# Performance work log

Measured on AMD Instinct MI355X. Metric: run time of the kernel, lower is better.

The kernel has to match this reference:

```python
import jax, jax.numpy as jnp
import numpy as np

N, E, D_IN, D, H = 50000, 600000, 128, 128, 128
NEG_SLOPE = 0.2  # PyG GATConv default


def setup_inputs() -> dict:
    key = jax.random.key(0)
    ks = jax.random.split(key, 10)
    s = 1.0 / np.sqrt(D)
    return {
        "x": jax.random.normal(ks[0], (N, D_IN), jnp.float32),
        "edge_index": jax.random.randint(ks[1], (2, E), 0, N, jnp.int64),
        "h": jax.random.normal(ks[2], (1, N, H), jnp.float32),
        "c": jax.random.normal(ks[3], (1, N, H), jnp.float32),
        "W": jax.random.normal(ks[4], (D_IN, D), jnp.float32) * s,
        "att_src": jax.random.normal(ks[5], (D,), jnp.float32) * s,
        "att_dst": jax.random.normal(ks[6], (D,), jnp.float32) * s,
        "bias_gat": jnp.zeros((D,), jnp.float32),
        "W_ih": jax.random.normal(ks[7], (4 * H, D), jnp.float32) * s,
        "W_hh": jax.random.normal(ks[8], (4 * H, H), jnp.float32) * s,
    }


def _gat_conv(x, edge_index, W, att_src, att_dst, bias_gat):
    n = x.shape[0]
    xs = x @ W  # [N, D]
    # add self loops (PyG default add_self_loops=True)
    loop = jnp.arange(n, dtype=edge_index.dtype)
    src = jnp.concatenate([edge_index[0], loop])
    dst = jnp.concatenate([edge_index[1], loop])
    a_src = xs @ att_src  # [N]
    a_dst = xs @ att_dst  # [N]
    e = a_src[src] + a_dst[dst]  # [E+N]
    e = jnp.where(e >= 0, e, NEG_SLOPE * e)  # leaky_relu
    # segment softmax over edges grouped by destination node
    e_max = jax.ops.segment_max(e, dst, num_segments=n)
    e_exp = jnp.exp(e - e_max[dst])
    e_sum = jax.ops.segment_sum(e_exp, dst, num_segments=n)
    alpha = e_exp / (e_sum[dst] + 1e-16)  # [E+N]
    out = jax.ops.segment_sum(alpha[:, None] * xs[src], dst, num_segments=n)
    return out + bias_gat


def _lstm_step(x, h0, c0, W_ih, W_hh):
    # torch LSTM gate order: i, f, g, o; bias=False
    gates = x @ W_ih.T + h0 @ W_hh.T  # [N, 4H]
    i, f, g, o = jnp.split(gates, 4, axis=-1)
    i, f, o = jax.nn.sigmoid(i), jax.nn.sigmoid(f), jax.nn.sigmoid(o)
    g = jnp.tanh(g)
    c1 = f * c0 + i * g
    h1 = o * jnp.tanh(c1)
    return h1, c1


def reference(x, edge_index, h, c, W, att_src, att_dst, bias_gat, W_ih, W_hh):
    xb = jnp.tanh(_gat_conv(x, edge_index, W, att_src, att_dst, bias_gat))  # [N, D]
    h1, c1 = _lstm_step(xb, h[0], c[0], W_ih, W_hh)
    # LSTM output for seq_len=1 equals the new hidden state
    return xb * 0 + h1, h1[None], c1[None]
```

## Files before the change

kernel.cpp:

```cpp
#include <hip/hip_runtime.h>
#include <hip/hip_bf16.h>
#include <math.h>

#define NEG 0.2f

typedef float f32x4 __attribute__((ext_vector_type(4)));
typedef short bf16x8 __attribute__((ext_vector_type(8)));

__device__ __forceinline__ float fsig(float x){ return 1.0f/(1.0f+__expf(-x)); }
__device__ __forceinline__ float ftanh(float x){ float e = __expf(2.0f*x); return 1.0f - 2.0f/(e+1.0f); }
__device__ __forceinline__ unsigned short f2bf(float v){
    __hip_bfloat16 b = __float2bfloat16(v);
    return *(unsigned short*)&b;
}
__device__ __forceinline__ bf16x8 pack8(float4 u, float4 v){
    bf16x8 r;
    r[0]=(short)f2bf(u.x); r[1]=(short)f2bf(u.y); r[2]=(short)f2bf(u.z); r[3]=(short)f2bf(u.w);
    r[4]=(short)f2bf(v.x); r[5]=(short)f2bf(v.y); r[6]=(short)f2bf(v.z); r[7]=(short)f2bf(v.w);
    return r;
}
__device__ __forceinline__ bf16x8 asbf(f32x4 v){ union{f32x4 f; bf16x8 h;} u; u.f=v; return u.h; }

__global__ void k_probe(const int* __restrict__ ei, int* __restrict__ flag){
    if(threadIdx.x==0){
        int nz=0;
        for(int i=0;i<64;i++) nz |= ei[2*i+1];
        *flag = (nz==0) ? 1 : 0;
    }
}

__global__ __launch_bounds__(256) void k_wpackx(const float* __restrict__ W,
                                                unsigned short* __restrict__ WPX){
    int f = blockIdx.x*256 + threadIdx.x;
    int l = f&63, ct = (f>>6)&7, ks = f>>9;
    int k0 = ks*32 + (l>>4)*8;
    int col = ct*16 + (l&15);
    #pragma unroll
    for(int j=0;j<8;j++) WPX[(size_t)f*8+j] = f2bf(W[(size_t)(k0+j)*128 + col]);
}

__global__ __launch_bounds__(256) void k_wtpack2(const float* __restrict__ W_ih,
                                                 const float* __restrict__ W_hh,
                                                 unsigned short* __restrict__ WP2){
    int f = blockIdx.x*256 + threadIdx.x;
    int l = f&63, ct = (f>>6)&3, ks = (f>>8)&7, g = f>>11;
    int k0 = ks*32 + (l>>4)*8;
    int col = ct*128 + g*16 + (l&15);
    #pragma unroll
    for(int j=0;j<8;j++){
        int k = k0+j;
        float w = (k<128) ? W_ih[(size_t)col*128+k] : W_hh[(size_t)col*128+(k-128)];
        WP2[(size_t)f*8+j] = f2bf(w);
    }
}

__global__ __launch_bounds__(256,2) void k_gemm_xs3(const float* __restrict__ x,
                                                    const unsigned short* __restrict__ WPX,
                                                    const float* __restrict__ att_s,
                                                    const float* __restrict__ att_d,
                                                    unsigned short* __restrict__ xsb,
                                                    float* __restrict__ a_src,
                                                    float* __restrict__ a_dst,
                                                    int n, int ntiles, int nwaves){
    const int w = threadIdx.x>>6, l = threadIdx.x&63;
    const int wid = blockIdx.x*4 + w;
    bf16x8 B[32];
    #pragma unroll
    for(int f=0;f<32;f++) B[f] = *(const bf16x8*)(WPX + (size_t)(f*64 + l)*8);
    float asv[8], adv[8];
    #pragma unroll
    for(int ct=0;ct<8;ct++){
        asv[ct] = att_s[ct*16 + (l&15)];
        adv[ct] = att_d[ct*16 + (l&15)];
    }
    for(int rt = wid; rt < ntiles; rt += nwaves){
        int arow = rt*16 + (l&15); if(arow>=n) arow = n-1;
        const float* xr = x + (size_t)arow*128 + (l>>4)*8;
        bf16x8 A[4];
        #pragma unroll
        for(int ks=0;ks<4;ks++){
            float4 u = *(const float4*)(xr + ks*32);
            float4 v = *(const float4*)(xr + ks*32 + 4);
            A[ks] = pack8(u,v);
        }
        f32x4 acc[8];
        #pragma unroll
        for(int ct=0;ct<8;ct++) acc[ct] = (f32x4){0.f,0.f,0.f,0.f};
        #pragma unroll
        for(int ks=0;ks<4;ks++){
            #pragma unroll
            for(int ct=0;ct<8;ct++)
                acc[ct] = __builtin_amdgcn_mfma_f32_16x16x32_bf16(A[ks], B[ks*8+ct], acc[ct], 0,0,0);
        }
        #pragma unroll
        for(int reg=0;reg<4;reg++){
            int row = rt*16 + (l>>4)*4 + reg;
            float ps=0.f, pd=0.f;
            #pragma unroll
            for(int ct=0;ct<8;ct++){ ps += acc[ct][reg]*asv[ct]; pd += acc[ct][reg]*adv[ct]; }
            ps += __shfl_xor(ps,1); pd += __shfl_xor(pd,1);
            ps += __shfl_xor(ps,2); pd += __shfl_xor(pd,2);
            ps += __shfl_xor(ps,4); pd += __shfl_xor(pd,4);
            ps += __shfl_xor(ps,8); pd += __shfl_xor(pd,8);
            if((l&15)==0 && row<n){ a_src[row]=ps; a_dst[row]=pd; }
            if(row<n){
                #pragma unroll
                for(int ct=0;ct<8;ct++)
                    xsb[(size_t)row*128 + ct*16 + (l&15)] = f2bf(acc[ct][reg]);
            }
        }
    }
}

__global__ __launch_bounds__(256) void k_hist(const int* __restrict__ ei,
                                              const int* __restrict__ flag,
                                              int* __restrict__ deg, int E, int EN){
    int e = blockIdx.x*256 + threadIdx.x;
    if(e>=EN) return;
    int dst = (e>=E) ? (e-E) : (*flag ? ei[2*(E+e)] : ei[E+e]);
    atomicAdd(&deg[dst], 1);
}

__global__ __launch_bounds__(256) void k_scan1(const int* __restrict__ deg,
                                               int* __restrict__ bsum, int n){
    __shared__ int ws[4];
    int b = blockIdx.x, t = threadIdx.x;
    int i = b*512 + t*2;
    int s = 0;
    if(i<n)   s += deg[i];
    if(i+1<n) s += deg[i+1];
    for(int off=32;off;off>>=1) s += __shfl_xor(s,off);
    if((t&63)==0) ws[t>>6]=s;
    __syncthreads();
    if(t==0) bsum[b]=ws[0]+ws[1]+ws[2]+ws[3];
}

__global__ void k_scan2(int* __restrict__ bsum, int* __restrict__ rowptr,
                        int nb, int n, int EN){
    int t = threadIdx.x;
    int v0 = (t<nb)    ? bsum[t]    : 0;
    int v1 = (64+t<nb) ? bsum[64+t] : 0;
    int x = v0;
    for(int d=1; d<64; d<<=1){ int y=__shfl_up(x,d); if(t>=d) x+=y; }
    int tot0 = __shfl(x,63);
    int x1 = v1;
    for(int d=1; d<64; d<<=1){ int y=__shfl_up(x1,d); if(t>=d) x1+=y; }
    if(t<nb)    bsum[t]    = x - v0;
    if(64+t<nb) bsum[64+t] = tot0 + x1 - v1;
    if(t==0) rowptr[n]=EN;
}

__global__ __launch_bounds__(256) void k_scan3(const int* __restrict__ deg,
                                               const int* __restrict__ bsum,
                                               int* __restrict__ rowptr,
                                               int* __restrict__ cursor, int n){
    __shared__ int wsum[4];
    int b = blockIdx.x, t = threadIdx.x;
    int i = b*512 + t*2;
    int d0 = (i<n)?deg[i]:0, d1 = (i+1<n)?deg[i+1]:0;
    int s = d0+d1;
    int x = s;
    int lane = t&63, wv = t>>6;
    for(int dd=1; dd<64; dd<<=1){ int y=__shfl_up(x,dd); if(lane>=dd) x+=y; }
    if(lane==63) wsum[wv]=x;
    __syncthreads();
    int woff=0;
    for(int w=0;w<wv;w++) woff += wsum[w];
    int ex = bsum[b] + woff + x - s;
    if(i<n)   { rowptr[i]  =ex;    cursor[i]  =ex;    }
    if(i+1<n) { rowptr[i+1]=ex+d0; cursor[i+1]=ex+d0; }
}

__global__ __launch_bounds__(256) void k_fill(const int* __restrict__ ei,
                                              const int* __restrict__ flag,
                                              int* __restrict__ cursor,
                                              int* __restrict__ csr_src, int E, int EN){
    int e = blockIdx.x*256 + threadIdx.x;
    if(e>=EN) return;
    int src,dst;
    if(e>=E){ src=dst=e-E; }
    else if(*flag){ src = ei[2*e]; dst = ei[2*(E+e)]; }
    else         { src = ei[e];   dst = ei[E+e]; }
    int pos = atomicAdd(&cursor[dst], 1);
    csr_src[pos] = src;
}

__global__ __launch_bounds__(256) void k_agg3(const int* __restrict__ rowptr,
                                              const int* __restrict__ csr_src,
                                              const float* __restrict__ a_src,
                                              const float* __restrict__ a_dst,
                                              const unsigned int* __restrict__ xsb32,
                                              const float* __restrict__ bg,
                                              const float* __restrict__ h0,
                                              unsigned short* __restrict__ xh, int n){
    const int wv = threadIdx.x>>6, l = threadIdx.x&63;
    const int dst = blockIdx.x*4 + wv;
    if(dst>=n) return;
    const int beg = rowptr[dst], end = rowptr[dst+1];
    const float ad = a_dst[dst];
    float ax=0.f, ay=0.f, psum=0.f;
    int j = beg;
    for(; j+8<=end; j+=8){
        int s0=csr_src[j],   s1=csr_src[j+1], s2=csr_src[j+2], s3=csr_src[j+3];
        int s4=csr_src[j+4], s5=csr_src[j+5], s6=csr_src[j+6], s7=csr_src[j+7];
        float e0=a_src[s0]+ad, e1=a_src[s1]+ad, e2=a_src[s2]+ad, e3=a_src[s3]+ad;
        float e4=a_src[s4]+ad, e5=a_src[s5]+ad, e6=a_src[s6]+ad, e7=a_src[s7]+ad;
        unsigned k0=xsb32[(size_t)s0*64+l], k1=xsb32[(size_t)s1*64+l];
        unsigned k2=xsb32[(size_t)s2*64+l], k3=xsb32[(size_t)s3*64+l];
        unsigned k4=xsb32[(size_t)s4*64+l], k5=xsb32[(size_t)s5*64+l];
        unsigned k6=xsb32[(size_t)s6*64+l], k7=xsb32[(size_t)s7*64+l];
        e0=e0>=0.f?e0:NEG*e0; e1=e1>=0.f?e1:NEG*e1; e2=e2>=0.f?e2:NEG*e2; e3=e3>=0.f?e3:NEG*e3;
        e4=e4>=0.f?e4:NEG*e4; e5=e5>=0.f?e5:NEG*e5; e6=e6>=0.f?e6:NEG*e6; e7=e7>=0.f?e7:NEG*e7;
        float p0=__expf(e0), p1=__expf(e1), p2=__expf(e2), p3=__expf(e3);
        float p4=__expf(e4), p5=__expf(e5), p6=__expf(e6), p7=__expf(e7);
        psum += (p0+p1+p2+p3)+(p4+p5+p6+p7);
        ax += p0*__uint_as_float(k0<<16) + p1*__uint_as_float(k1<<16)
            + p2*__uint_as_float(k2<<16) + p3*__uint_as_float(k3<<16)
            + p4*__uint_as_float(k4<<16) + p5*__uint_as_float(k5<<16)
            + p6*__uint_as_float(k6<<16) + p7*__uint_as_float(k7<<16);
        ay += p0*__uint_as_float(k0&0xffff0000u) + p1*__uint_as_float(k1&0xffff0000u)
            + p2*__uint_as_float(k2&0xffff0000u) + p3*__uint_as_float(k3&0xffff0000u)
            + p4*__uint_as_float(k4&0xffff0000u) + p5*__uint_as_float(k5&0xffff0000u)
            + p6*__uint_as_float(k6&0xffff0000u) + p7*__uint_as_float(k7&0xffff0000u);
    }
    for(; j<end; ++j){
        int s = csr_src[j];
        float sv = a_src[s]+ad;
        sv = sv>=0.f ? sv : NEG*sv;
        float p = __expf(sv);
        psum += p;
        unsigned pk = xsb32[(size_t)s*64 + l];
        ax += p*__uint_as_float(pk<<16);
        ay += p*__uint_as_float(pk & 0xffff0000u);
    }
    const float inv = 1.0f/(psum + 1e-16f);
    float t0 = ftanh(ax*inv + bg[2*l]);
    float t1 = ftanh(ay*inv + bg[2*l+1]);
    unsigned int pk = (unsigned)f2bf(t0) | ((unsigned)f2bf(t1)<<16);
    unsigned int* xr = (unsigned int*)(xh + (size_t)dst*256);
    xr[l] = pk;
    float2 hv = *(const float2*)(h0 + (size_t)dst*128 + 2*l);
    xr[64 + l] = (unsigned)f2bf(hv.x) | ((unsigned)f2bf(hv.y)<<16);
}

__global__ __launch_bounds__(256,2) void k_lstm8(const unsigned short* __restrict__ xh,
                                                 const unsigned short* __restrict__ WP2,
                                                 const float* __restrict__ c0,
                                                 float* __restrict__ out,
                                                 int n, int ntiles, int wstride){
    const int t = threadIdx.x;
    const int w = t>>6, l = t&63;
    const int wid = blockIdx.x*4 + w;
    const int g = wid & 7, wgi = wid >> 3;
    const unsigned short* wp = WP2 + (size_t)g*16384;
    f32x4 B[32];
    #pragma unroll
    for(int f=0;f<32;f++) B[f] = *(const f32x4*)(wp + (size_t)(f*64 + l)*8);
    #pragma unroll
    for(int f=0;f<32;f++) asm volatile("" : "+v"(B[f]));
    const size_t nn = (size_t)n*128;
    const int col = g*16 + (l&15);
    int rt = wgi;
    if(rt >= ntiles) return;
    bf16x8 A[8]; float cc[4];
    {
        int arow = rt*16 + (l&15); if(arow>=n) arow=n-1;
        const unsigned short* ar = xh + (size_t)arow*256 + (l>>4)*8;
        #pragma unroll
        for(int ks=0;ks<8;ks++) A[ks] = *(const bf16x8*)(ar + ks*32);
        int rbase = rt*16 + (l>>4)*4;
        #pragma unroll
        for(int r=0;r<4;r++){ int rr=rbase+r; if(rr>=n) rr=n-1; cc[r]=c0[(size_t)rr*128+col]; }
    }
    while(rt < ntiles){
        const int rtn = rt + wstride;
        bf16x8 A2[8]; float cc2[4];
        if(rtn < ntiles){
            int arow = rtn*16 + (l&15); if(arow>=n) arow=n-1;
            const unsigned short* ar = xh + (size_t)arow*256 + (l>>4)*8;
            #pragma unroll
            for(int ks=0;ks<8;ks++) A2[ks] = *(const bf16x8*)(ar + ks*32);
            int rbase = rtn*16 + (l>>4)*4;
            #pragma unroll
            for(int r=0;r<4;r++){ int rr=rbase+r; if(rr>=n) rr=n-1; cc2[r]=c0[(size_t)rr*128+col]; }
        }
        f32x4 acc[4];
        #pragma unroll
        for(int ct=0;ct<4;ct++) acc[ct] = (f32x4){0.f,0.f,0.f,0.f};
        #pragma unroll
        for(int ks=0;ks<8;ks++){
            #pragma unroll
            for(int ct=0;ct<4;ct++)
                acc[ct] = __builtin_amdgcn_mfma_f32_16x16x32_bf16(A[ks], asbf(B[ks*4+ct]), acc[ct], 0,0,0);
        }
        #pragma unroll
        for(int reg=0;reg<4;reg++){
            int row = rt*16 + (l>>4)*4 + reg;
            if(row>=n) continue;
            float gi=acc[0][reg], gf=acc[1][reg], gg=acc[2][reg], go=acc[3][reg];
            float c1v = fsig(gf)*cc[reg] + fsig(gi)*ftanh(gg);
            float h1v = fsig(go)*ftanh(c1v);
            __builtin_nontemporal_store(h1v, &out[(size_t)row*128+col]);
            __builtin_nontemporal_store(h1v, &out[nn + (size_t)row*128+col]);
            __builtin_nontemporal_store(c1v, &out[2*nn + (size_t)row*128+col]);
        }
        rt = rtn;
        if(rt < ntiles){
            #pragma unroll
            for(int ks=0;ks<8;ks++) A[ks] = A2[ks];
            #pragma unroll
            for(int r=0;r<4;r++) cc[r] = cc2[r];
        }
    }
}

extern "C" void kernel_launch(void* const* d_in, const int* in_sizes, int n_in,
                              void* d_out, int out_size, void* d_ws, size_t ws_size,
                              hipStream_t stream) {
    const float* x      = (const float*)d_in[0];
    const int*   ei     = (const int*)  d_in[1];
    const float* h      = (const float*)d_in[2];
    const float* c      = (const float*)d_in[3];
    const float* W      = (const float*)d_in[4];
    const float* atts   = (const float*)d_in[5];
    const float* attd   = (const float*)d_in[6];
    const float* bias   = (const float*)d_in[7];
    const float* W_ih   = (const float*)d_in[8];
    const float* W_hh   = (const float*)d_in[9];
    float* out = (float*)d_out;

    const int n  = in_sizes[0]/128;
    const int E  = in_sizes[1]/2;
    const int EN = E + n;
    const int NB = (n + 511)/512;
    const int ntiles = (n + 15)/16;
    const int n2 = ntiles*16;

    unsigned short* xsb = (unsigned short*)d_ws;
    unsigned short* xh  = xsb + (size_t)n*128;
    unsigned short* WP2 = xh + (size_t)n2*256;
    unsigned short* WPX = WP2 + 131072;
    float* a_src = (float*)(WPX + 16384);
    float* a_dst = a_src + n;
    int*   deg    = (int*)(a_dst + n);
    int*   rowptr = deg + n;
    int*   cursor = rowptr + n + 1;
    int*   bsum   = cursor + n;
    int*   csr_src= bsum + 128;
    int*   flag   = csr_src + EN;

    hipMemsetAsync(deg, 0, (size_t)n*sizeof(int), stream);
    k_probe<<<1,64,0,stream>>>(ei, flag);
    k_wpackx<<<8,256,0,stream>>>(W, WPX);
    k_wtpack2<<<64,256,0,stream>>>(W_ih, W_hh, WP2);
    k_gemm_xs3<<<1024,256,0,stream>>>(x, WPX, atts, attd, xsb, a_src, a_dst, n, ntiles, 4096);
    k_hist<<<(EN+255)/256,256,0,stream>>>(ei,flag,deg,E,EN);
    k_scan1<<<NB,256,0,stream>>>(deg,bsum,n);
    k_scan2<<<1,64,0,stream>>>(bsum,rowptr,NB,n,EN);
    k_scan3<<<NB,256,0,stream>>>(deg,bsum,rowptr,cursor,n);
    k_fill<<<(EN+255)/256,256,0,stream>>>(ei,flag,cursor,csr_src,E,EN);
    k_agg3<<<(n+3)/4,256,0,stream>>>(rowptr,csr_src,a_src,a_dst,(const unsigned int*)xsb,bias,h,xh,n);
    k_lstm8<<<1024,256,0,stream>>>(xh, WP2, c, out, n, ntiles, 512);
}
```

Before: 180.4 us.

## Restructure LSTM GEMM to stage weights in LDS and loop gate groups per tile

The LSTM GEMM kernel used to pin one gate-column group's weights in registers, with each wave grid-striding over row tiles and prefetching the next tile. Now each wave owns a single 16-row tile and keeps its A fragments in registers. The block loops over all 8 column groups, staging each group's 32KB weight slice into shared memory behind barriers. This lowers register pressure (launch bounds go from 2 to 4 blocks) and reads the xh rows once instead of 8 times. In exchange it adds 16 barriers per block, reloads the weights from global memory per block, and drops the nontemporal stores and the software prefetch.

Measured after the change: 173.8 us. 3.7% less time.

```diff
diff --git a/kernel.cpp b/kernel.cpp
--- a/kernel.cpp
+++ b/kernel.cpp
@@ -19,7 +19,6 @@
     r[4]=(short)f2bf(v.x); r[5]=(short)f2bf(v.y); r[6]=(short)f2bf(v.z); r[7]=(short)f2bf(v.w);
     return r;
 }
-__device__ __forceinline__ bf16x8 asbf(f32x4 v){ union{f32x4 f; bf16x8 h;} u; u.f=v; return u.h; }
 
 __global__ void k_probe(const int* __restrict__ ei, int* __restrict__ flag){
     if(threadIdx.x==0){
@@ -243,73 +242,60 @@
     xr[64 + l] = (unsigned)f2bf(hv.x) | ((unsigned)f2bf(hv.y)<<16);
 }
 
-__global__ __launch_bounds__(256,2) void k_lstm8(const unsigned short* __restrict__ xh,
+__global__ __launch_bounds__(256,4) void k_lstm9(const unsigned short* __restrict__ xh,
                                                  const unsigned short* __restrict__ WP2,
                                                  const float* __restrict__ c0,
                                                  float* __restrict__ out,
-                                                 int n, int ntiles, int wstride){
+                                                 int n, int ntiles){
+    __shared__ unsigned short Bl[16384];
     const int t = threadIdx.x;
     const int w = t>>6, l = t&63;
-    const int wid = blockIdx.x*4 + w;
-    const int g = wid & 7, wgi = wid >> 3;
-    const unsigned short* wp = WP2 + (size_t)g*16384;
-    f32x4 B[32];
-    #pragma unroll
-    for(int f=0;f<32;f++) B[f] = *(const f32x4*)(wp + (size_t)(f*64 + l)*8);
-    #pragma unroll
-    for(int f=0;f<32;f++) asm volatile("" : "+v"(B[f]));
+    const int rt = blockIdx.x*4 + w;
     const size_t nn = (size_t)n*128;
-    const int col = g*16 + (l&15);
-    int rt = wgi;
-    if(rt >= ntiles) return;
-    bf16x8 A[8]; float cc[4];
-    {
+    const bool live = (rt < ntiles);
+    bf16x8 A[8];
+    if(live){
         int arow = rt*16 + (l&15); if(arow>=n) arow=n-1;
         const unsigned short* ar = xh + (size_t)arow*256 + (l>>4)*8;
         #pragma unroll
         for(int ks=0;ks<8;ks++) A[ks] = *(const bf16x8*)(ar + ks*32);
-        int rbase = rt*16 + (l>>4)*4;
+    }
+    const int rbase = rt*16 + (l>>4)*4;
+    for(int g=0; g<8; ++g){
+        __syncthreads();
+        {
+            const float4* gsrc = (const float4*)(WP2 + (size_t)g*16384);
+            float4* ldst = (float4*)Bl;
+            #pragma unroll
+            for(int i=0;i<8;i++) ldst[t + i*256] = gsrc[t + i*256];
+        }
+        __syncthreads();
+        if(!live) continue;
+        const int col = g*16 + (l&15);
+        float cc[4];
         #pragma unroll
         for(int r=0;r<4;r++){ int rr=rbase+r; if(rr>=n) rr=n-1; cc[r]=c0[(size_t)rr*128+col]; }
-    }
-    while(rt < ntiles){
-        const int rtn = rt + wstride;
-        bf16x8 A2[8]; float cc2[4];
-        if(rtn < ntiles){
-            int arow = rtn*16 + (l&15); if(arow>=n) arow=n-1;
-            const unsigned short* ar = xh + (size_t)arow*256 + (l>>4)*8;
-            #pragma unroll
-            for(int ks=0;ks<8;ks++) A2[ks] = *(const bf16x8*)(ar + ks*32);
-            int rbase = rtn*16 + (l>>4)*4;
-            #pragma unroll
-            for(int r=0;r<4;r++){ int rr=rbase+r; if(rr>=n) rr=n-1; cc2[r]=c0[(size_t)rr*128+col]; }
-        }
         f32x4 acc[4];
         #pragma unroll
         for(int ct=0;ct<4;ct++) acc[ct] = (f32x4){0.f,0.f,0.f,0.f};
         #pragma unroll
         for(int ks=0;ks<8;ks++){
             #pragma unroll
-            for(int ct=0;ct<4;ct++)
-                acc[ct] = __builtin_amdgcn_mfma_f32_16x16x32_bf16(A[ks], asbf(B[ks*4+ct]), acc[ct], 0,0,0);
+            for(int ct=0;ct<4;ct++){
+                const bf16x8 b = *(const bf16x8*)(Bl + ((ks*4+ct)*64 + l)*8);
+                acc[ct] = __builtin_amdgcn_mfma_f32_16x16x32_bf16(A[ks], b, acc[ct], 0,0,0);
+            }
         }
         #pragma unroll
         for(int reg=0;reg<4;reg++){
-            int row = rt*16 + (l>>4)*4 + reg;
+            int row = rbase + reg;
             if(row>=n) continue;
             float gi=acc[0][reg], gf=acc[1][reg], gg=acc[2][reg], go=acc[3][reg];
             float c1v = fsig(gf)*cc[reg] + fsig(gi)*ftanh(gg);
             float h1v = fsig(go)*ftanh(c1v);
-            __builtin_nontemporal_store(h1v, &out[(size_t)row*128+col]);
-            __builtin_nontemporal_store(h1v, &out[nn + (size_t)row*128+col]);
-            __builtin_nontemporal_store(c1v, &out[2*nn + (size_t)row*128+col]);
-        }
-        rt = rtn;
-        if(rt < ntiles){
-            #pragma unroll
-            for(int ks=0;ks<8;ks++) A[ks] = A2[ks];
-            #pragma unroll
-            for(int r=0;r<4;r++) cc[r] = cc2[r];
+            out[(size_t)row*128+col]        = h1v;
+            out[nn + (size_t)row*128+col]   = h1v;
+            out[2*nn + (size_t)row*128+col] = c1v;
         }
     }
 }
@@ -360,5 +346,5 @@
     k_scan3<<<NB,256,0,stream>>>(deg,bsum,rowptr,cursor,n);
     k_fill<<<(EN+255)/256,256,0,stream>>>(ei,flag,cursor,csr_src,E,EN);
     k_agg3<<<(n+3)/4,256,0,stream>>>(rowptr,csr_src,a_src,a_dst,(const unsigned int*)xsb,bias,h,xh,n);
-    k_lstm8<<<1024,256,0,stream>>>(xh, WP2, c, out, n, ntiles, 512);
-}
+    k_lstm9<<<(ntiles+3)/4,256,0,stream>>>(xh, WP2, c, out, n, ntiles);
+}
```
